# Optimization experiments

Hardware: AMD Instinct MI355X
Metric: run time of the kernel (lower is better)

Reference implementation:

```python
import jax, jax.numpy as jnp
import numpy as np

NT, NB, NY = 1200, 16384, 8
W_LOW, W_HIGH = 0.2, 1.75  # seasonal weights: months 6..9 get W_HIGH


def setup_inputs() -> dict:
    key = jax.random.key(0)
    k1, k2 = jax.random.split(key)
    output = jax.random.normal(k1, (NT, NB, NY), dtype=jnp.float32)
    target = jax.random.normal(k2, (NT, NB, NY), dtype=jnp.float32)
    return {"output": output, "target": target}


def reference(output, target):
    nt = target.shape[0]
    mon = jnp.arange(nt) % 12
    w = jnp.where((mon >= 6) & (mon <= 9), W_HIGH, W_LOW).astype(output.dtype)  # [nt]
    dif = (output - target) * w[:, None, None]  # [nt, nb, ny]
    # per-channel weighted RMSE, summed over channels
    loss = jnp.sqrt(jnp.mean(dif * dif, axis=(0, 1))).sum()
    return loss
```

## Files before the change

kernel.cpp:

```cpp
#include <hip/hip_runtime.h>
#include <hip/hip_bf16.h>
#include <math.h>

#define NT 1200
#define NB 16384
#define NY 8
#define NGROUPS (NT * NB)
#define NQ      (NT * NB * NY / 4)
#define GRID    1536
#define BLOCK   256
#define NTHREADS (GRID * BLOCK)
#define CHUNK   4
#define NITER   (NQ / (NTHREADS * CHUNK))
#define W_LOW  0.2f
#define W_HIGH 1.75f

typedef float f32x4 __attribute__((ext_vector_type(4)));

__global__ __launch_bounds__(BLOCK) void rmse_partial_kernel(
    const float* __restrict__ outp, const float* __restrict__ tgtp,
    float* __restrict__ ws)
{
    const f32x4* __restrict__ o4 = reinterpret_cast<const f32x4*>(outp);
    const f32x4* __restrict__ t4 = reinterpret_cast<const f32x4*>(tgtp);

    const int c0 = blockIdx.x * BLOCK + threadIdx.x;

    f32x4 accA = {0.0f, 0.0f, 0.0f, 0.0f};
    f32x4 accB = {0.0f, 0.0f, 0.0f, 0.0f};

#pragma unroll 1
    for (int it = 0; it < NITER; ++it) {
        const int c   = c0 + it * NTHREADS;
        const int qb  = c << 2;
        const int t   = c >> 13;
        const int mon = t % 12;
        const float w2 = (mon >= 6 && mon <= 9) ? (W_HIGH * W_HIGH)
                                                : (W_LOW * W_LOW);

        f32x4 a0 = o4[qb + 0];
        f32x4 a1 = o4[qb + 1];
        f32x4 a2 = o4[qb + 2];
        f32x4 a3 = o4[qb + 3];
        f32x4 b0 = t4[qb + 0];
        f32x4 b1 = t4[qb + 1];
        f32x4 b2 = t4[qb + 2];
        f32x4 b3 = t4[qb + 3];

        f32x4 d0 = a0 - b0;
        f32x4 d1 = a1 - b1;
        f32x4 d2 = a2 - b2;
        f32x4 d3 = a3 - b3;

        accA += (w2 * d0) * d0;
        accB += (w2 * d1) * d1;
        accA += (w2 * d2) * d2;
        accB += (w2 * d3) * d3;
    }

#pragma unroll
    for (int mask = 1; mask <= 32; mask <<= 1) {
        accA.x += __shfl_xor(accA.x, mask, 64);
        accA.y += __shfl_xor(accA.y, mask, 64);
        accA.z += __shfl_xor(accA.z, mask, 64);
        accA.w += __shfl_xor(accA.w, mask, 64);
        accB.x += __shfl_xor(accB.x, mask, 64);
        accB.y += __shfl_xor(accB.y, mask, 64);
        accB.z += __shfl_xor(accB.z, mask, 64);
        accB.w += __shfl_xor(accB.w, mask, 64);
    }

    __shared__ float sh[4][NY];
    const int wave = threadIdx.x >> 6;
    const int lane = threadIdx.x & 63;
    if (lane == 0) {
        sh[wave][0] = accA.x; sh[wave][1] = accA.y;
        sh[wave][2] = accA.z; sh[wave][3] = accA.w;
        sh[wave][4] = accB.x; sh[wave][5] = accB.y;
        sh[wave][6] = accB.z; sh[wave][7] = accB.w;
    }
    __syncthreads();

    if (threadIdx.x < NY) {
        const int ch = threadIdx.x;
        float s = sh[0][ch] + sh[1][ch] + sh[2][ch] + sh[3][ch];
        atomicAdd(&ws[ch], s);
    }
}

__global__ void rmse_final_kernel(const float* __restrict__ ws, float* __restrict__ out)
{
    if (threadIdx.x == 0 && blockIdx.x == 0) {
        const float inv_n = 1.0f / (float)NGROUPS;
        float s = 0.0f;
#pragma unroll
        for (int c = 0; c < NY; ++c)
            s += sqrtf(ws[c] * inv_n);
        out[0] = s;
    }
}

extern "C" void kernel_launch(void* const* d_in, const int* in_sizes, int n_in,
                              void* d_out, int out_size, void* d_ws, size_t ws_size,
                              hipStream_t stream) {
    const float* outp = (const float*)d_in[0];
    const float* tgtp = (const float*)d_in[1];
    float* ws  = (float*)d_ws;
    float* out = (float*)d_out;

    (void)hipMemsetAsync(ws, 0, NY * sizeof(float), stream);

    rmse_partial_kernel<<<GRID, BLOCK, 0, stream>>>(outp, tgtp, ws);
    rmse_final_kernel<<<1, 64, 0, stream>>>(ws, out);
}
```

Before: 213.6 us.

## Double per-thread chunk, halve grid, replace atomics with two-stage deterministic reduction

```diff
diff --git a/kernel.cpp b/kernel.cpp
--- a/kernel.cpp
+++ b/kernel.cpp
@@ -7,10 +7,10 @@
 #define NY 8
 #define NGROUPS (NT * NB)
 #define NQ      (NT * NB * NY / 4)
-#define GRID    1536
+#define GRID    768
 #define BLOCK   256
 #define NTHREADS (GRID * BLOCK)
-#define CHUNK   4
+#define CHUNK   8
 #define NITER   (NQ / (NTHREADS * CHUNK))
 #define W_LOW  0.2f
 #define W_HIGH 1.75f
@@ -32,30 +32,25 @@
 #pragma unroll 1
     for (int it = 0; it < NITER; ++it) {
         const int c   = c0 + it * NTHREADS;
-        const int qb  = c << 2;
-        const int t   = c >> 13;
+        const int qb  = c << 3;
+        const int t   = c >> 12;
         const int mon = t % 12;
         const float w2 = (mon >= 6 && mon <= 9) ? (W_HIGH * W_HIGH)
                                                 : (W_LOW * W_LOW);
 
-        f32x4 a0 = o4[qb + 0];
-        f32x4 a1 = o4[qb + 1];
-        f32x4 a2 = o4[qb + 2];
-        f32x4 a3 = o4[qb + 3];
-        f32x4 b0 = t4[qb + 0];
-        f32x4 b1 = t4[qb + 1];
-        f32x4 b2 = t4[qb + 2];
-        f32x4 b3 = t4[qb + 3];
+        f32x4 a[CHUNK], b[CHUNK];
+#pragma unroll
+        for (int u = 0; u < CHUNK; ++u) a[u] = o4[qb + u];
+#pragma unroll
+        for (int u = 0; u < CHUNK; ++u) b[u] = t4[qb + u];
 
-        f32x4 d0 = a0 - b0;
-        f32x4 d1 = a1 - b1;
-        f32x4 d2 = a2 - b2;
-        f32x4 d3 = a3 - b3;
-
-        accA += (w2 * d0) * d0;
-        accB += (w2 * d1) * d1;
-        accA += (w2 * d2) * d2;
-        accB += (w2 * d3) * d3;
+#pragma unroll
+        for (int u = 0; u < CHUNK; u += 2) {
+            f32x4 dA = a[u]     - b[u];
+            f32x4 dB = a[u + 1] - b[u + 1];
+            accA += (w2 * dA) * dA;
+            accB += (w2 * dB) * dB;
+        }
     }
 
 #pragma unroll
@@ -83,20 +78,39 @@
 
     if (threadIdx.x < NY) {
         const int ch = threadIdx.x;
-        float s = sh[0][ch] + sh[1][ch] + sh[2][ch] + sh[3][ch];
-        atomicAdd(&ws[ch], s);
+        ws[blockIdx.x * NY + ch] = sh[0][ch] + sh[1][ch] + sh[2][ch] + sh[3][ch];
     }
 }
 
-__global__ void rmse_final_kernel(const float* __restrict__ ws, float* __restrict__ out)
+__global__ __launch_bounds__(256) void rmse_final_kernel(
+    const float* __restrict__ ws, float* __restrict__ out)
 {
-    if (threadIdx.x == 0 && blockIdx.x == 0) {
+    const int ch    = threadIdx.x & 7;
+    const int slice = threadIdx.x >> 3;
+
+    float s = 0.0f;
+    for (int j = slice; j < GRID; j += 32)
+        s += ws[j * NY + ch];
+
+    s += __shfl_xor(s, 8, 64);
+    s += __shfl_xor(s, 16, 64);
+    s += __shfl_xor(s, 32, 64);
+
+    __shared__ float sh[4][NY];
+    const int wave = threadIdx.x >> 6;
+    const int lane = threadIdx.x & 63;
+    if (lane < NY) sh[wave][lane] = s;
+    __syncthreads();
+
+    if (threadIdx.x == 0) {
         const float inv_n = 1.0f / (float)NGROUPS;
-        float s = 0.0f;
+        float total = 0.0f;
 #pragma unroll
-        for (int c = 0; c < NY; ++c)
-            s += sqrtf(ws[c] * inv_n);
-        out[0] = s;
+        for (int c = 0; c < NY; ++c) {
+            float v = sh[0][c] + sh[1][c] + sh[2][c] + sh[3][c];
+            total += sqrtf(v * inv_n);
+        }
+        out[0] = total;
     }
 }
 
@@ -108,8 +122,6 @@
     float* ws  = (float*)d_ws;
     float* out = (float*)d_out;
 
-    (void)hipMemsetAsync(ws, 0, NY * sizeof(float), stream);
-
     rmse_partial_kernel<<<GRID, BLOCK, 0, stream>>>(outp, tgtp, ws);
-    rmse_final_kernel<<<1, 64, 0, stream>>>(ws, out);
+    rmse_final_kernel<<<1, 256, 0, stream>>>(ws, out);
 }
```

Measured after the change: 305.1 us. 42.9% more time.
